# Optimization experiments

Measured on AMD Instinct MI355X. Metric: run time of the kernel, lower is better.

The kernel has to match this reference:

```python
import jax, jax.numpy as jnp
import numpy as np

B, S = 4, 128
N_ITERS = 3  # original hardcodes range(3) regardless of max_iter


def _build_masks(edge_mask, chart_mask):
    S_ = edge_mask.shape[-1]
    ar = jnp.arange(S_)
    ne = ar[:, None] != ar[None, :]          # [a,b]: a != b
    le = ar[:, None] <= ar[None, :]
    ge = ar[:, None] >= ar[None, :]
    ls = jnp.minimum(ar[:, None], ar[None, :])  # min(a,b)
    rs = jnp.maximum(ar[:, None], ar[None, :])  # max(a,b)

    # edge_mask2o[b,h,m,s] = edge_mask[b,h,s] & edge_mask[b,h,m] & (m != s)
    em2o = edge_mask[:, :, None, :] & edge_mask[:, :, :, None]
    em2o = em2o & ne[None, None, :, :]
    # lrhs[h,m,s] = (min(m,s) >= h) | (max(m,s) <= h)
    lrhs = (ls[None, :, :] >= ar[:, None, None]) | (rs[None, :, :] <= ar[:, None, None])
    noncross = em2o & lrhs[None]
    # additionally require h != s for plain edge_mask2o
    em2o = em2o & ne[:, None, :][None]

    cm0 = chart_mask[:, 0]                                  # [B,S]
    pad = cm0[:, :, None] & cm0[:, None, :]                 # [B,S,S]
    chart_r = jnp.roll(chart_mask, 1, axis=1)               # cat((cm[:,-1:], cm[:,:-1]))
    # span_mask2o[b,i,j,s] = chart_r[b,i,j] & pad[b,j,s] & (max(i,j) != s)
    span2o = chart_r[:, :, :, None] & pad[:, None, :, :]
    span2o = span2o & (rs[:, :, None] != ar[None, None, :])[None]
    # inside[i,j,s] = (i <= s) & (j >= s)
    inside = le[:, None, :] & ge[None, :, :]
    outside = (~inside)[None] & span2o
    # off-diagonal pad mask: pad.triu(1) | pad.tril(-1) == pad & (i != j)
    outside = outside & (pad & ne[None])[:, :, :, None]
    return em2o, noncross, span2o, outside


def setup_inputs() -> dict:
    key = jax.random.key(0)
    ks = jax.random.split(key, 12)
    lens = jax.random.randint(ks[0], (B,), S // 2, S)
    valid = jnp.arange(S)[None, :] < lens[:, None]          # [B,S]
    edge_mask = valid[:, :, None] & valid[:, None, :]
    tri = jnp.triu(jnp.ones((S, S), dtype=bool), 1)
    chart_mask = edge_mask & tri[None]
    def rn(k, shape):
        return jax.random.normal(k, shape, dtype=jnp.float32)
    return {
        's_edge': rn(ks[1], (B, S, S)),
        's_const': rn(ks[2], (B, S, S)),
        's_sib': rn(ks[3], (B, S, S, S)),
        's_cop': rn(ks[4], (B, S, S, S)),
        's_grd': rn(ks[5], (B, S, S, S)),
        's_end_point': rn(ks[6], (B, S, S, S)),
        's_split': rn(ks[7], (B, S, S, S)),
        's_head_span_b': rn(ks[8], (B, S, S, S)),
        's_head_span_e': rn(ks[9], (B, S, S, S)),
        'edge_mask': edge_mask,
        'chart_mask': chart_mask,
    }


def reference(s_edge, s_const, s_sib, s_cop, s_grd, s_end_point, s_split,
              s_head_span_b, s_head_span_e, edge_mask, chart_mask):
    # symmetrize span scores: triu + triu(1).T on last two dims
    s_span = jnp.triu(s_const) + jnp.swapaxes(jnp.triu(s_const, 1), -1, -2)
    em2o, noncross, span2o, outside = _build_masks(edge_mask, chart_mask)

    s_sib = s_sib * em2o
    s_cop = s_cop * em2o
    s_grd = s_grd * em2o
    s_end_point = s_end_point * noncross
    s_split = s_split * span2o
    s_hb = s_head_span_b * outside
    s_he = jnp.transpose(s_head_span_e, (0, 2, 1, 3)) * outside

    # Note: the torch code aliases tmp_q_edge to s_edge and uses +=, so the
    # base scores accumulate across iterations; equivalently q <- q + update.
    q_edge, q_span = s_edge, s_span
    for _ in range(N_ITERS):
        pe = jax.nn.sigmoid(q_edge)
        ps = jax.nn.sigmoid(q_span)
        upd_e = (jnp.einsum('bhs,bhms->bhm', pe, s_sib)
                 + jnp.einsum('bsm,bhms->bhm', pe, s_cop)
                 + jnp.einsum('bms,bhms->bhm', ps, s_grd)
                 + jnp.einsum('bms,bhms->bhm', ps, s_end_point))
        upd_s = (jnp.einsum('bis,bijs->bis', ps, s_split)
                 + jnp.einsum('bsi,bijs->bij', pe, s_hb)
                 + jnp.einsum('bsj,bijs->bij', pe, s_he))
        q_edge = q_edge + upd_e
        q_span = q_span + upd_s
    return q_edge, q_span
```

## Files before the change

kernel.cpp:

```cpp
#include <hip/hip_runtime.h>
#include <stdint.h>

#define BB 4
#define SDIM 128
#define S2 (SDIM*SDIM)
#define S3 ((size_t)SDIM*S2)


__global__ void k_valid(const void* __restrict__ em, int* __restrict__ lens) {
    const int t = threadIdx.x;
    __shared__ int s_ok;
    __shared__ int s_v[SDIM];
    if (t == 0) s_ok = 1;
    __syncthreads();
    const unsigned char* p8 = (const unsigned char*)em;
    for (int b = 0; b < BB; ++b) {
        unsigned char v = p8[(size_t)b*S2 + (size_t)t*SDIM + t];
        if ((t < SDIM/2 && !v) || (t == SDIM-1 && v)) atomicAnd(&s_ok, 0);
    }
    __syncthreads();
    const int use8 = s_ok;
    const int* p32 = (const int*)em;
    for (int b = 0; b < BB; ++b) {
        size_t idx = (size_t)b*S2 + (size_t)t*SDIM + t;
        s_v[t] = use8 ? (p8[idx] != 0) : (p32[idx] != 0);
        __syncthreads();
        if (t == 0) { int L = 0; for (int k = 0; k < SDIM; ++k) L += s_v[k]; lens[b] = L; }
        __syncthreads();
    }
}

__global__ void k_init(const float* __restrict__ s_edge, const float* __restrict__ s_const,
                       float* __restrict__ q_edge, float* __restrict__ q_span) {
    int blk = blockIdx.x; int b = blk / SDIM; int i = blk % SDIM; int t = threadIdx.x;
    size_t ro = (size_t)b*S2 + (size_t)i*SDIM;
    q_edge[ro + t] = s_edge[ro + t];
    float v = (i <= t) ? s_const[ro + t] : s_const[(size_t)b*S2 + (size_t)t*SDIM + i];
    q_span[ro + t] = v;
}

__global__ __launch_bounds__(256) void k_split(const float* __restrict__ s_split,
                                               const int* __restrict__ lens,
                                               float* __restrict__ splitsum) {
    const int b = blockIdx.x / SDIM, i = blockIdx.x % SDIM;
    const int len = lens[b];
    const int t = threadIdx.x;
    float* out = splitsum + (size_t)b*S2 + (size_t)i*SDIM;
    if (i < 1 || i >= len) { if (t < SDIM) out[t] = 0.f; return; }
    const int g = t >> 5;
    const int kq = (t & 31) * 4;
    const float* base = s_split + (size_t)b*S3 + (size_t)i*S2;
    float4 acc = make_float4(0.f, 0.f, 0.f, 0.f);
    int j = i + g;
    for (; j + 8 < len; j += 16) {
        float4 v0 = *(const float4*)(base + (size_t)j*SDIM + kq);
        float4 v1 = *(const float4*)(base + (size_t)(j+8)*SDIM + kq);
        acc.x += ((j   != kq+0) ? v0.x : 0.f) + ((j+8 != kq+0) ? v1.x : 0.f);
        acc.y += ((j   != kq+1) ? v0.y : 0.f) + ((j+8 != kq+1) ? v1.y : 0.f);
        acc.z += ((j   != kq+2) ? v0.z : 0.f) + ((j+8 != kq+2) ? v1.z : 0.f);
        acc.w += ((j   != kq+3) ? v0.w : 0.f) + ((j+8 != kq+3) ? v1.w : 0.f);
    }
    if (j < len) {
        float4 v0 = *(const float4*)(base + (size_t)j*SDIM + kq);
        acc.x += (j != kq+0) ? v0.x : 0.f;
        acc.y += (j != kq+1) ? v0.y : 0.f;
        acc.z += (j != kq+2) ? v0.z : 0.f;
        acc.w += (j != kq+3) ? v0.w : 0.f;
    }
    __shared__ float red[8][SDIM];
    *(float4*)&red[g][kq] = acc;
    __syncthreads();
    if (t < SDIM) {
        float s = 0.f;
        #pragma unroll
        for (int gg = 0; gg < 8; ++gg) s += red[gg][t];
        out[t] = (t >= 1 && t < len) ? s : 0.f;
    }
}

__global__ void k_sig(const float* __restrict__ q_edge, const float* __restrict__ q_span,
                      float* __restrict__ pe, float* __restrict__ peT, float* __restrict__ ps) {
    int blk = blockIdx.x; int b = blk / SDIM; int r = blk % SDIM; int t = threadIdx.x;
    size_t o = (size_t)b*S2 + (size_t)r*SDIM + t;
    float v = 1.f / (1.f + expf(-q_edge[o]));
    pe[o] = v;
    peT[(size_t)b*S2 + (size_t)t*SDIM + r] = v;
    ps[o] = 1.f / (1.f + expf(-q_span[o]));
}

__global__ __launch_bounds__(256) void k_upde(
    const float* __restrict__ s_sib, const float* __restrict__ s_cop,
    const float* __restrict__ s_grd, const float* __restrict__ s_ep,
    const float* __restrict__ pe, const float* __restrict__ peT,
    const float* __restrict__ ps, const int* __restrict__ lens,
    float* __restrict__ q_edge) {
    const int b = blockIdx.x / SDIM, h = blockIdx.x % SDIM;
    const int len = lens[b];
    if (h >= len) return;
    const int m0 = blockIdx.y * 32;
    if (m0 >= len) return;
    const int tid = threadIdx.x, wave = tid >> 6, lane = tid & 63;
    const int half = lane >> 5, sq = (lane & 31) * 4;
    const size_t vb = (size_t)b*S2;
    const size_t tb = (size_t)b*S3 + (size_t)h*S2;
    const float4 pe4 = *(const float4*)(pe + vb + (size_t)h*SDIM + sq);
    #pragma unroll
    for (int it = 0; it < 4; ++it) {
        const int me = m0 + 8*it + 2*wave;
        if (me >= len) continue;
        const int m = me + half;
        const bool mv = (m < len);
        const size_t ro = tb + (size_t)m*SDIM + sq;
        float4 sib4 = *(const float4*)(s_sib + ro);
        float4 cop4 = *(const float4*)(s_cop + ro);
        float4 grd4 = *(const float4*)(s_grd + ro);
        float4 ep4  = *(const float4*)(s_ep  + ro);
        const size_t vo = vb + (size_t)m*SDIM + sq;
        float4 peT4 = *(const float4*)(peT + vo);
        float4 ps4  = *(const float4*)(ps  + vo);
        float r = 0.f;
        #define TERM(C, F) { const int s = sq + C;                                   \
            const bool bs = mv && (s < len) && (m != s);                             \
            const float fem = (bs && (h != s)) ? 1.f : 0.f;                          \
            const float fnc = (bs && ((m >= h && s >= h) || (m <= h && s <= h)))     \
                              ? 1.f : 0.f;                                           \
            r += fem * (sib4.F*pe4.F + cop4.F*peT4.F + grd4.F*ps4.F)                 \
               + fnc * (ep4.F*ps4.F); }
        TERM(0, x) TERM(1, y) TERM(2, z) TERM(3, w)
        #undef TERM
        r += __shfl_xor(r, 16); r += __shfl_xor(r, 8); r += __shfl_xor(r, 4);
        r += __shfl_xor(r, 2);  r += __shfl_xor(r, 1);
        if ((lane & 31) == 0 && mv)
            q_edge[vb + (size_t)h*SDIM + m] += r;
    }
}

__global__ __launch_bounds__(256) void k_upds(
    const float* __restrict__ s_hb, const float* __restrict__ s_he,
    const float* __restrict__ peT, const float* __restrict__ ps,
    const float* __restrict__ splitsum, const int* __restrict__ lens,
    float* __restrict__ q_span) {
    const int b = blockIdx.x / SDIM, i = blockIdx.x % SDIM;
    const int len = lens[b];
    if (i < 1 || i >= len) return;
    const int j0 = blockIdx.y * 32;
    if (j0 >= len) return;
    const int tid = threadIdx.x, wave = tid >> 6, lane = tid & 63;
    const int half = lane >> 5, sq = (lane & 31) * 4;
    const size_t vb = (size_t)b*S2;
    const float4 peTi4 = *(const float4*)(peT + vb + (size_t)i*SDIM + sq);
    #pragma unroll
    for (int it = 0; it < 4; ++it) {
        const int je = j0 + 8*it + 2*wave;
        if (je >= len) continue;
        const int j = je + half;
        const bool jv = (j >= 1 && j < len);
        const bool act = (j > i) && (j < len);
        const bool anyact = (je + 1 > i);
        float r = 0.f;
        if (anyact) {
            const size_t hbo = (size_t)b*S3 + (size_t)i*S2 + (size_t)j*SDIM + sq;
            const size_t heo = (size_t)b*S3 + (size_t)j*S2 + (size_t)i*SDIM + sq;
            float4 hb4 = *(const float4*)(s_hb + hbo);
            float4 he4 = *(const float4*)(s_he + heo);
            float4 peTj4 = *(const float4*)(peT + vb + (size_t)j*SDIM + sq);
            #define TERM(C, F) { const int s = sq + C;                               \
                const float f = (act && s >= 1 && s < len && (s < i || s > j))       \
                                ? 1.f : 0.f;                                         \
                r += f * (hb4.F*peTi4.F + he4.F*peTj4.F); }
            TERM(0, x) TERM(1, y) TERM(2, z) TERM(3, w)
            #undef TERM
            r += __shfl_xor(r, 16); r += __shfl_xor(r, 8); r += __shfl_xor(r, 4);
            r += __shfl_xor(r, 2);  r += __shfl_xor(r, 1);
        }
        if ((lane & 31) == 0 && jv) {
            const size_t qo = vb + (size_t)i*SDIM + j;
            q_span[qo] += r + ps[qo] * splitsum[qo];
        }
    }
}

extern "C" void kernel_launch(void* const* d_in, const int* in_sizes, int n_in,
                              void* d_out, int out_size, void* d_ws, size_t ws_size,
                              hipStream_t stream) {
    const float* s_edge  = (const float*)d_in[0];
    const float* s_const = (const float*)d_in[1];
    const float* s_sib   = (const float*)d_in[2];
    const float* s_cop   = (const float*)d_in[3];
    const float* s_grd   = (const float*)d_in[4];
    const float* s_ep    = (const float*)d_in[5];
    const float* s_split = (const float*)d_in[6];
    const float* s_hb    = (const float*)d_in[7];
    const float* s_he    = (const float*)d_in[8];
    const void*  em      = d_in[9];
    (void)in_sizes; (void)n_in; (void)out_size; (void)ws_size;

    float* q_edge = (float*)d_out;
    float* q_span = q_edge + (size_t)BB * S2;

    char* ws = (char*)d_ws;
    int*   lens     = (int*)(ws + 0);
    float* splitsum = (float*)(ws + 256);
    float* pe       = (float*)(ws + 256 + 1*(size_t)BB*S2*sizeof(float));
    float* peT      = (float*)(ws + 256 + 2*(size_t)BB*S2*sizeof(float));
    float* ps       = (float*)(ws + 256 + 3*(size_t)BB*S2*sizeof(float));

    const int NB = BB * SDIM;
    hipLaunchKernelGGL(k_valid, dim3(1), dim3(SDIM), 0, stream, em, lens);
    hipLaunchKernelGGL(k_init,  dim3(NB), dim3(SDIM), 0, stream, s_edge, s_const, q_edge, q_span);
    hipLaunchKernelGGL(k_split, dim3(NB), dim3(256), 0, stream, s_split, lens, splitsum);
    for (int it = 0; it < 3; ++it) {
        hipLaunchKernelGGL(k_sig,  dim3(NB), dim3(SDIM), 0, stream, q_edge, q_span, pe, peT, ps);
        hipLaunchKernelGGL(k_upde, dim3(dim3(NB, 4)), dim3(256), 0, stream,
                           s_sib, s_cop, s_grd, s_ep, pe, peT, ps, lens, q_edge);
        hipLaunchKernelGGL(k_upds, dim3(dim3(NB, 4)), dim3(256), 0, stream,
                           s_hb, s_he, peT, ps, splitsum, lens, q_span);
    }
}
```

Baseline: 292.0 us.

## Fuse prep kernels and merge edge/span updates into one launch per iteration

Replaces the separate length-probe, init and split kernels with one prep kernel that computes sequence lengths inline via wave ballots. The edge and span update kernels become a single launch with a doubled grid, where the y index selects the path. Loads are also skipped when the column block lies beyond len. This removes launch overhead and serialization between small kernels, at the cost of every block recomputing the length probe.

```diff
diff --git a/kernel.cpp b/kernel.cpp
--- a/kernel.cpp
+++ b/kernel.cpp
@@ -6,75 +6,66 @@
 #define S2 (SDIM*SDIM)
 #define S3 ((size_t)SDIM*S2)
 
-
-__global__ void k_valid(const void* __restrict__ em, int* __restrict__ lens) {
-    const int t = threadIdx.x;
-    __shared__ int s_ok;
-    __shared__ int s_v[SDIM];
-    if (t == 0) s_ok = 1;
-    __syncthreads();
+__device__ __forceinline__ int probe_len(const void* em, int b, int lane) {
     const unsigned char* p8 = (const unsigned char*)em;
-    for (int b = 0; b < BB; ++b) {
-        unsigned char v = p8[(size_t)b*S2 + (size_t)t*SDIM + t];
-        if ((t < SDIM/2 && !v) || (t == SDIM-1 && v)) atomicAnd(&s_ok, 0);
-    }
-    __syncthreads();
-    const int use8 = s_ok;
     const int* p32 = (const int*)em;
-    for (int b = 0; b < BB; ++b) {
-        size_t idx = (size_t)b*S2 + (size_t)t*SDIM + t;
-        s_v[t] = use8 ? (p8[idx] != 0) : (p32[idx] != 0);
-        __syncthreads();
-        if (t == 0) { int L = 0; for (int k = 0; k < SDIM; ++k) L += s_v[k]; lens[b] = L; }
-        __syncthreads();
-    }
-}
-
-__global__ void k_init(const float* __restrict__ s_edge, const float* __restrict__ s_const,
-                       float* __restrict__ q_edge, float* __restrict__ q_span) {
-    int blk = blockIdx.x; int b = blk / SDIM; int i = blk % SDIM; int t = threadIdx.x;
-    size_t ro = (size_t)b*S2 + (size_t)i*SDIM;
-    q_edge[ro + t] = s_edge[ro + t];
-    float v = (i <= t) ? s_const[ro + t] : s_const[(size_t)b*S2 + (size_t)t*SDIM + i];
-    q_span[ro + t] = v;
-}
-
-__global__ __launch_bounds__(256) void k_split(const float* __restrict__ s_split,
-                                               const int* __restrict__ lens,
-                                               float* __restrict__ splitsum) {
-    const int b = blockIdx.x / SDIM, i = blockIdx.x % SDIM;
-    const int len = lens[b];
-    const int t = threadIdx.x;
-    float* out = splitsum + (size_t)b*S2 + (size_t)i*SDIM;
-    if (i < 1 || i >= len) { if (t < SDIM) out[t] = 0.f; return; }
-    const int g = t >> 5;
-    const int kq = (t & 31) * 4;
-    const float* base = s_split + (size_t)b*S3 + (size_t)i*S2;
+    const int t0 = lane, t1 = lane + 64;
+    const size_t i0 = (size_t)b*S2 + (size_t)t0*SDIM + t0;
+    const size_t i1 = (size_t)b*S2 + (size_t)t1*SDIM + t1;
+    const unsigned char a0 = p8[i0], a1 = p8[i1];
+    const bool ok = (a0 != 0) && (t1 != SDIM-1 || a1 == 0);
+    const unsigned long long mok = __ballot(ok);
+    const bool use8 = (mok == ~0ull);
+    int v0, v1;
+    if (use8) { v0 = (a0 != 0); v1 = (a1 != 0); }
+    else      { v0 = (p32[i0] != 0); v1 = (p32[i1] != 0); }
+    return __popcll(__ballot(v0)) + __popcll(__ballot(v1));
+}
+
+__global__ __launch_bounds__(256) void k_prep(
+    const float* __restrict__ s_edge, const float* __restrict__ s_const,
+    const float* __restrict__ s_split, const void* __restrict__ em,
+    float* __restrict__ q_edge, float* __restrict__ q_span,
+    float* __restrict__ splitsum) {
+    const int b = blockIdx.x >> 7, i = blockIdx.x & 127;
+    const int tid = threadIdx.x, lane = tid & 63;
+    const int len = probe_len(em, b, lane);
+    const size_t vb = (size_t)b*S2;
+    if (tid < SDIM) {
+        const size_t ro = vb + (size_t)i*SDIM + tid;
+        q_edge[ro] = s_edge[ro];
+        q_span[ro] = (i <= tid) ? s_const[ro] : s_const[vb + (size_t)tid*SDIM + i];
+    }
+    const int g = tid >> 5;
+    const int kq = (tid & 31) * 4;
     float4 acc = make_float4(0.f, 0.f, 0.f, 0.f);
-    int j = i + g;
-    for (; j + 8 < len; j += 16) {
-        float4 v0 = *(const float4*)(base + (size_t)j*SDIM + kq);
-        float4 v1 = *(const float4*)(base + (size_t)(j+8)*SDIM + kq);
-        acc.x += ((j   != kq+0) ? v0.x : 0.f) + ((j+8 != kq+0) ? v1.x : 0.f);
-        acc.y += ((j   != kq+1) ? v0.y : 0.f) + ((j+8 != kq+1) ? v1.y : 0.f);
-        acc.z += ((j   != kq+2) ? v0.z : 0.f) + ((j+8 != kq+2) ? v1.z : 0.f);
-        acc.w += ((j   != kq+3) ? v0.w : 0.f) + ((j+8 != kq+3) ? v1.w : 0.f);
-    }
-    if (j < len) {
-        float4 v0 = *(const float4*)(base + (size_t)j*SDIM + kq);
-        acc.x += (j != kq+0) ? v0.x : 0.f;
-        acc.y += (j != kq+1) ? v0.y : 0.f;
-        acc.z += (j != kq+2) ? v0.z : 0.f;
-        acc.w += (j != kq+3) ? v0.w : 0.f;
+    if (i >= 1 && i < len && kq < len) {
+        const float* base = s_split + (size_t)b*S3 + (size_t)i*S2;
+        int j = i + g;
+        for (; j + 8 < len; j += 16) {
+            float4 v0 = *(const float4*)(base + (size_t)j*SDIM + kq);
+            float4 v1 = *(const float4*)(base + (size_t)(j+8)*SDIM + kq);
+            acc.x += ((j   != kq+0) ? v0.x : 0.f) + ((j+8 != kq+0) ? v1.x : 0.f);
+            acc.y += ((j   != kq+1) ? v0.y : 0.f) + ((j+8 != kq+1) ? v1.y : 0.f);
+            acc.z += ((j   != kq+2) ? v0.z : 0.f) + ((j+8 != kq+2) ? v1.z : 0.f);
+            acc.w += ((j   != kq+3) ? v0.w : 0.f) + ((j+8 != kq+3) ? v1.w : 0.f);
+        }
+        if (j < len) {
+            float4 v0 = *(const float4*)(base + (size_t)j*SDIM + kq);
+            acc.x += (j != kq+0) ? v0.x : 0.f;
+            acc.y += (j != kq+1) ? v0.y : 0.f;
+            acc.z += (j != kq+2) ? v0.z : 0.f;
+            acc.w += (j != kq+3) ? v0.w : 0.f;
+        }
     }
     __shared__ float red[8][SDIM];
     *(float4*)&red[g][kq] = acc;
     __syncthreads();
-    if (t < SDIM) {
+    if (tid < SDIM) {
         float s = 0.f;
         #pragma unroll
-        for (int gg = 0; gg < 8; ++gg) s += red[gg][t];
-        out[t] = (t >= 1 && t < len) ? s : 0.f;
+        for (int gg = 0; gg < 8; ++gg) s += red[gg][tid];
+        splitsum[vb + (size_t)i*SDIM + tid] = (tid >= 1 && tid < len) ? s : 0.f;
     }
 }
 
@@ -88,94 +79,89 @@
     ps[o] = 1.f / (1.f + expf(-q_span[o]));
 }
 
-__global__ __launch_bounds__(256) void k_upde(
+__global__ __launch_bounds__(256) void k_upd(
     const float* __restrict__ s_sib, const float* __restrict__ s_cop,
     const float* __restrict__ s_grd, const float* __restrict__ s_ep,
+    const float* __restrict__ s_hb,  const float* __restrict__ s_he,
     const float* __restrict__ pe, const float* __restrict__ peT,
-    const float* __restrict__ ps, const int* __restrict__ lens,
-    float* __restrict__ q_edge) {
-    const int b = blockIdx.x / SDIM, h = blockIdx.x % SDIM;
-    const int len = lens[b];
-    if (h >= len) return;
-    const int m0 = blockIdx.y * 32;
-    if (m0 >= len) return;
+    const float* __restrict__ ps, const float* __restrict__ splitsum,
+    const void* __restrict__ em,
+    float* __restrict__ q_edge, float* __restrict__ q_span) {
+    const int b = blockIdx.x >> 7, row = blockIdx.x & 127;
     const int tid = threadIdx.x, wave = tid >> 6, lane = tid & 63;
     const int half = lane >> 5, sq = (lane & 31) * 4;
+    const int len = probe_len(em, b, lane);
     const size_t vb = (size_t)b*S2;
-    const size_t tb = (size_t)b*S3 + (size_t)h*S2;
-    const float4 pe4 = *(const float4*)(pe + vb + (size_t)h*SDIM + sq);
-    #pragma unroll
-    for (int it = 0; it < 4; ++it) {
-        const int me = m0 + 8*it + 2*wave;
-        if (me >= len) continue;
-        const int m = me + half;
-        const bool mv = (m < len);
-        const size_t ro = tb + (size_t)m*SDIM + sq;
-        float4 sib4 = *(const float4*)(s_sib + ro);
-        float4 cop4 = *(const float4*)(s_cop + ro);
-        float4 grd4 = *(const float4*)(s_grd + ro);
-        float4 ep4  = *(const float4*)(s_ep  + ro);
-        const size_t vo = vb + (size_t)m*SDIM + sq;
-        float4 peT4 = *(const float4*)(peT + vo);
-        float4 ps4  = *(const float4*)(ps  + vo);
-        float r = 0.f;
-        #define TERM(C, F) { const int s = sq + C;                                   \
-            const bool bs = mv && (s < len) && (m != s);                             \
-            const float fem = (bs && (h != s)) ? 1.f : 0.f;                          \
-            const float fnc = (bs && ((m >= h && s >= h) || (m <= h && s <= h)))     \
-                              ? 1.f : 0.f;                                           \
-            r += fem * (sib4.F*pe4.F + cop4.F*peT4.F + grd4.F*ps4.F)                 \
-               + fnc * (ep4.F*ps4.F); }
-        TERM(0, x) TERM(1, y) TERM(2, z) TERM(3, w)
-        #undef TERM
-        r += __shfl_xor(r, 16); r += __shfl_xor(r, 8); r += __shfl_xor(r, 4);
-        r += __shfl_xor(r, 2);  r += __shfl_xor(r, 1);
-        if ((lane & 31) == 0 && mv)
-            q_edge[vb + (size_t)h*SDIM + m] += r;
-    }
-}
-
-__global__ __launch_bounds__(256) void k_upds(
-    const float* __restrict__ s_hb, const float* __restrict__ s_he,
-    const float* __restrict__ peT, const float* __restrict__ ps,
-    const float* __restrict__ splitsum, const int* __restrict__ lens,
-    float* __restrict__ q_span) {
-    const int b = blockIdx.x / SDIM, i = blockIdx.x % SDIM;
-    const int len = lens[b];
-    if (i < 1 || i >= len) return;
-    const int j0 = blockIdx.y * 32;
-    if (j0 >= len) return;
-    const int tid = threadIdx.x, wave = tid >> 6, lane = tid & 63;
-    const int half = lane >> 5, sq = (lane & 31) * 4;
-    const size_t vb = (size_t)b*S2;
-    const float4 peTi4 = *(const float4*)(peT + vb + (size_t)i*SDIM + sq);
-    #pragma unroll
-    for (int it = 0; it < 4; ++it) {
-        const int je = j0 + 8*it + 2*wave;
-        if (je >= len) continue;
-        const int j = je + half;
-        const bool jv = (j >= 1 && j < len);
-        const bool act = (j > i) && (j < len);
-        const bool anyact = (je + 1 > i);
-        float r = 0.f;
-        if (anyact) {
-            const size_t hbo = (size_t)b*S3 + (size_t)i*S2 + (size_t)j*SDIM + sq;
-            const size_t heo = (size_t)b*S3 + (size_t)j*S2 + (size_t)i*SDIM + sq;
-            float4 hb4 = *(const float4*)(s_hb + hbo);
-            float4 he4 = *(const float4*)(s_he + heo);
-            float4 peTj4 = *(const float4*)(peT + vb + (size_t)j*SDIM + sq);
-            #define TERM(C, F) { const int s = sq + C;                               \
-                const float f = (act && s >= 1 && s < len && (s < i || s > j))       \
-                                ? 1.f : 0.f;                                         \
-                r += f * (hb4.F*peTi4.F + he4.F*peTj4.F); }
-            TERM(0, x) TERM(1, y) TERM(2, z) TERM(3, w)
-            #undef TERM
+
+    if (blockIdx.y < 4) {
+        const int h = row;
+        if (h >= len) return;
+        const int m0 = blockIdx.y * 32;
+        if (m0 >= len) return;
+        const size_t tb = (size_t)b*S3 + (size_t)h*S2;
+        const float4 pe4 = *(const float4*)(pe + vb + (size_t)h*SDIM + sq);
+        #pragma unroll
+        for (int it = 0; it < 4; ++it) {
+            const int me = m0 + 8*it + 2*wave;
+            if (me >= len) continue;
+            const int m = me + half;
+            const bool mv = (m < len);
+            float r = 0.f;
+            if (mv && sq < len) {
+                const size_t ro = tb + (size_t)m*SDIM + sq;
+                const float4 sib4 = *(const float4*)(s_sib + ro);
+                const float4 cop4 = *(const float4*)(s_cop + ro);
+                const float4 grd4 = *(const float4*)(s_grd + ro);
+                const float4 ep4  = *(const float4*)(s_ep  + ro);
+                const size_t vo = vb + (size_t)m*SDIM + sq;
+                const float4 peT4 = *(const float4*)(peT + vo);
+                const float4 ps4  = *(const float4*)(ps  + vo);
+                #define TERM(C, F) { const int s = sq + C;                               \
+                    const bool bs = (s < len) && (m != s);                               \
+                    const float fem = (bs && (h != s)) ? 1.f : 0.f;                      \
+                    const float fnc = (bs && ((m >= h && s >= h) || (m <= h && s <= h))) \
+                                      ? 1.f : 0.f;                                       \
+                    r += fem * (sib4.F*pe4.F + cop4.F*peT4.F + grd4.F*ps4.F)             \
+                       + fnc * (ep4.F*ps4.F); }
+                TERM(0, x) TERM(1, y) TERM(2, z) TERM(3, w)
+                #undef TERM
+            }
             r += __shfl_xor(r, 16); r += __shfl_xor(r, 8); r += __shfl_xor(r, 4);
             r += __shfl_xor(r, 2);  r += __shfl_xor(r, 1);
-        }
-        if ((lane & 31) == 0 && jv) {
-            const size_t qo = vb + (size_t)i*SDIM + j;
-            q_span[qo] += r + ps[qo] * splitsum[qo];
+            if ((lane & 31) == 0 && mv)
+                q_edge[vb + (size_t)h*SDIM + m] += r;
+        }
+    } else {
+        const int i = row;
+        if (i < 1 || i >= len) return;
+        const int j0 = (blockIdx.y - 4) * 32;
+        if (j0 >= len) return;
+        const float4 peTi4 = *(const float4*)(peT + vb + (size_t)i*SDIM + sq);
+        #pragma unroll
+        for (int it = 0; it < 4; ++it) {
+            const int je = j0 + 8*it + 2*wave;
+            if (je >= len) continue;
+            const int j = je + half;
+            const bool jv = (j >= 1 && j < len);
+            float r = 0.f;
+            if (j > i && j < len && sq < len) {
+                const size_t hbo = (size_t)b*S3 + (size_t)i*S2 + (size_t)j*SDIM + sq;
+                const size_t heo = (size_t)b*S3 + (size_t)j*S2 + (size_t)i*SDIM + sq;
+                const float4 hb4 = *(const float4*)(s_hb + hbo);
+                const float4 he4 = *(const float4*)(s_he + heo);
+                const float4 peTj4 = *(const float4*)(peT + vb + (size_t)j*SDIM + sq);
+                #define TERM(C, F) { const int s = sq + C;                               \
+                    const float f = (s >= 1 && s < len && (s < i || s > j)) ? 1.f : 0.f; \
+                    r += f * (hb4.F*peTi4.F + he4.F*peTj4.F); }
+                TERM(0, x) TERM(1, y) TERM(2, z) TERM(3, w)
+                #undef TERM
+            }
+            r += __shfl_xor(r, 16); r += __shfl_xor(r, 8); r += __shfl_xor(r, 4);
+            r += __shfl_xor(r, 2);  r += __shfl_xor(r, 1);
+            if ((lane & 31) == 0 && jv) {
+                const size_t qo = vb + (size_t)i*SDIM + j;
+                q_span[qo] += r + ps[qo] * splitsum[qo];
+            }
         }
     }
 }
@@ -199,21 +185,18 @@
     float* q_span = q_edge + (size_t)BB * S2;
 
     char* ws = (char*)d_ws;
-    int*   lens     = (int*)(ws + 0);
-    float* splitsum = (float*)(ws + 256);
-    float* pe       = (float*)(ws + 256 + 1*(size_t)BB*S2*sizeof(float));
-    float* peT      = (float*)(ws + 256 + 2*(size_t)BB*S2*sizeof(float));
-    float* ps       = (float*)(ws + 256 + 3*(size_t)BB*S2*sizeof(float));
+    float* splitsum = (float*)(ws);
+    float* pe       = (float*)(ws + 1*(size_t)BB*S2*sizeof(float));
+    float* peT      = (float*)(ws + 2*(size_t)BB*S2*sizeof(float));
+    float* ps       = (float*)(ws + 3*(size_t)BB*S2*sizeof(float));
 
     const int NB = BB * SDIM;
-    hipLaunchKernelGGL(k_valid, dim3(1), dim3(SDIM), 0, stream, em, lens);
-    hipLaunchKernelGGL(k_init,  dim3(NB), dim3(SDIM), 0, stream, s_edge, s_const, q_edge, q_span);
-    hipLaunchKernelGGL(k_split, dim3(NB), dim3(256), 0, stream, s_split, lens, splitsum);
+    hipLaunchKernelGGL(k_prep, dim3(NB), dim3(256), 0, stream,
+                       s_edge, s_const, s_split, em, q_edge, q_span, splitsum);
     for (int it = 0; it < 3; ++it) {
-        hipLaunchKernelGGL(k_sig,  dim3(NB), dim3(SDIM), 0, stream, q_edge, q_span, pe, peT, ps);
-        hipLaunchKernelGGL(k_upde, dim3(dim3(NB, 4)), dim3(256), 0, stream,
-                           s_sib, s_cop, s_grd, s_ep, pe, peT, ps, lens, q_edge);
-        hipLaunchKernelGGL(k_upds, dim3(dim3(NB, 4)), dim3(256), 0, stream,
-                           s_hb, s_he, peT, ps, splitsum, lens, q_span);
-    }
-}
+        hipLaunchKernelGGL(k_sig, dim3(NB), dim3(SDIM), 0, stream, q_edge, q_span, pe, peT, ps);
+        hipLaunchKernelGGL(k_upd, dim3(dim3(NB, 8)), dim3(256), 0, stream,
+                           s_sib, s_cop, s_grd, s_ep, s_hb, s_he,
+                           pe, peT, ps, splitsum, em, q_edge, q_span);
+    }
+}
```

Measured after the change: 286.3 us. -2.0%, faster.
